# Optimization experiments

Measured on AMD Instinct MI355X. Metric: run time of the kernel, lower is better.

Reference implementation:

```python
import jax, jax.numpy as jnp
import numpy as np
from jax import lax

T = 3650      # days
H = 256       # MLP hidden width
N_IN = 4      # [s_snow, s_water, prcp, tmean]
N_OUT = 5     # [p_snow, p_rain, m, et, q]
DT = 1.0      # euler step (days), equals forcing sampling interval


def setup_inputs() -> dict:
    key = jax.random.key(0)
    ks = jax.random.split(key, 8)
    # inputs[:, 0]=s_snow init traj, [:,1]=s_water, [:,2]=prcp, [:,3]=tmean, [:,4]=time
    data = jax.random.normal(ks[0], (T, 4), dtype=jnp.float32)
    data = data.at[:, 2].set(jnp.abs(data[:, 2]))  # prcp >= 0
    time = jnp.arange(T, dtype=jnp.float32)[:, None]
    inputs = jnp.concatenate([data, time], axis=-1)  # [T, 5]
    dayl = jax.random.uniform(ks[1], (T,), dtype=jnp.float32)  # day length fraction
    s = 0.1  # small init keeps sinh/exp transforms stable over the long rollout
    W0 = jax.random.normal(ks[2], (N_IN, H), dtype=jnp.float32) * (s / np.sqrt(N_IN))
    b0 = jnp.zeros((H,), dtype=jnp.float32)
    W1 = jax.random.normal(ks[3], (H, H), dtype=jnp.float32) * (s / np.sqrt(H))
    b1 = jnp.zeros((H,), dtype=jnp.float32)
    W2 = jax.random.normal(ks[4], (H, H), dtype=jnp.float32) * (s / np.sqrt(H))
    b2 = jnp.zeros((H,), dtype=jnp.float32)
    Wout = jax.random.normal(ks[5], (H, N_OUT), dtype=jnp.float32) * (s / np.sqrt(H))
    bout = jnp.zeros((N_OUT,), dtype=jnp.float32)
    return {"inputs": inputs, "dayl": dayl, "W0": W0, "b0": b0, "W1": W1,
            "b1": b1, "W2": W2, "b2": b2, "Wout": Wout, "bout": bout}


def _step_function(x):
    return (jnp.tanh(5.0 * x) + 1.0) * 0.5


def reference(inputs, dayl, W0, b0, W1, b1, W2, b2, Wout, bout):
    prcp = inputs[:, 2]
    tmean = inputs[:, 3]
    s_snow0 = inputs[0, 0]
    s_water0 = inputs[0, 1]

    def mlp(x):  # x: [..., N_IN] -> [..., N_OUT]
        h = jnp.tanh(x @ W0 + b0)
        h = jnp.tanh(h @ W1 + b1)
        h = jnpp_tanh(h @ W2 + b2) if False else jnp.tanh(h @ W2 + b2)
        return h @ Wout + bout

    def derivs(s0, s1, p, tm, ld):
        o = mlp(jnp.stack([s0, s1, p, tm]))  # [5]
        p_snow, p_rain, m, et, q = o[0], o[1], o[2], o[3], o[4]
        # scale_target_vars transform path
        p_snow = jax.nn.relu(jnp.sinh(p_snow) * _step_function(-tm))
        p_rain = jax.nn.relu(jnp.sinh(p_rain))
        m = jax.nn.relu(_step_function(s0) * jnp.sinh(m))
        et = _step_function(s1) * jnp.exp(et) * ld
        q = _step_function(s1) * jnp.exp(q)
        return p_snow - m, p_rain + m - et - q

    def body(carry, xs):
        s0, s1 = carry
        p, tm, ld = xs
        d0, d1 = derivs(s0, s1, p, tm, ld)
        ns0 = s0 + DT * d0
        ns1 = s1 + DT * d1
        return (ns0, ns1), (ns0, ns1)

    xs = (prcp[:-1], tmean[:-1], dayl[:-1])
    _, (ss, sw) = lax.scan(body, (s_snow0, s_water0), xs)
    s_snow_nn = jnp.concatenate([s_snow0[None], ss])    # [T]
    s_water_nn = jnp.concatenate([s_water0[None], sw])  # [T]

    inputs_nn = jnp.stack([s_snow_nn, s_water_nn, prcp, tmean], axis=-1)  # [T, 4]
    q_output = mlp(inputs_nn)[:, -1]  # last head = q
    return (q_output, s_snow_nn, s_water_nn)
```

## Files before the change

### kernel.cpp

```cpp
#include <hip/hip_runtime.h>
#include <hip/hip_bf16.h>

#define TT 3650
#define HH 256

typedef _Float16 f16x4 __attribute__((ext_vector_type(4)));
typedef _Float16 f16x8 __attribute__((ext_vector_type(8)));
typedef float f32x4 __attribute__((ext_vector_type(4)));

__device__ __forceinline__ float xexp2(float x) { return __builtin_amdgcn_exp2f(x); }
__device__ __forceinline__ float xrcp(float x) { return __builtin_amdgcn_rcpf(x); }
__device__ __forceinline__ float xexp(float x) { return xexp2(x * 1.4426950408889634f); }
__device__ __forceinline__ float xtanh(float x) {
  float e = xexp2(x * 2.8853900817779268f);
  return 1.0f - 2.0f * xrcp(e + 1.0f);
}
__device__ __forceinline__ float xtanh_ds(float d) {
  float e = xexp2(d * 0.0028177637517362566f);
  return 1.0f - 2.0f * xrcp(e + 1.0f);
}
__device__ __forceinline__ float xstep(float x) {
  return xrcp(1.0f + xexp2(-14.426950408889634f * x));
}
__device__ __forceinline__ float xsinh(float x) {
  float e = xexp(x);
  return 0.5f * (e - xrcp(e));
}

#define DPPADD(x, ctrl)                                                        \
  (x) += __builtin_bit_cast(float, __builtin_amdgcn_update_dpp(                \
            0, __builtin_bit_cast(int, (x)), (ctrl), 0xf, 0xf, false));
#define RDLANE(x, l)                                                           \
  __builtin_bit_cast(float,                                                    \
      __builtin_amdgcn_readlane(__builtin_bit_cast(int, (x)), (l)))

#define REP8(M) M(0) M(1) M(2) M(3) M(4) M(5) M(6) M(7)
#define REPC(M) M(0) M(1) M(2) M(3)

#define WSCALE 1024.0f

#define SF_PAD 2

__global__ void __launch_bounds__(256, 1) exphydro_scan(
    const float* __restrict__ gin, const float* __restrict__ gdayl,
    const float* __restrict__ gW0, const float* __restrict__ gb0,
    const float* __restrict__ gW1, const float* __restrict__ gb1,
    const float* __restrict__ gW2, const float* __restrict__ gb2,
    const float* __restrict__ gWout, const float* __restrict__ gbout,
    float* __restrict__ gout) {
  __shared__ alignas(16) _Float16 h0l[HH];
  __shared__ alignas(16) _Float16 h1l[HH];
  __shared__ float sWP[64];
  __shared__ f32x4 sF[TT + SF_PAD];
  __shared__ float sQ[TT], sS0[TT], sS1[TT];

  const int tid = threadIdx.x;
  const int lane = tid & 63;
  const int w = tid >> 6;
  const int li = lane & 15;
  const int g = lane >> 4;
  const int jb = 64 * w + 4 * li;
  const int j0 = 64 * w + lane;

  for (int i = tid; i < TT; i += 256) {
    f32x4 F = {gin[5 * i + 2], gin[5 * i + 3], gdayl[i], 0.0f};
    sF[i] = F;
  }
  if (tid < SF_PAD) {
    f32x4 Z = {0.f, 0.f, 0.f, 0.f};
    sF[TT + tid] = Z;
  }
  if (tid < 64) sWP[tid] = 0.0f;

  float s0 = gin[0], s1 = gin[1];
  const float bo0 = gbout[0], bo1 = gbout[1], bo2 = gbout[2], bo3 = gbout[3],
              bo4 = gbout[4];
  const float w00J = gW0[j0], w01J = gW0[HH + j0], w02J = gW0[2 * HH + j0],
              w03J = gW0[3 * HH + j0], b0J = gb0[j0];
#define CDECL(c)                                                               \
  const float b1s_##c = gb1[jb + (c)] * WSCALE,                                \
              b2s_##c = gb2[jb + (c)] * WSCALE,                                \
              wo0_##c = gWout[5 * (jb + (c)) + 0],                             \
              wo1_##c = gWout[5 * (jb + (c)) + 1],                             \
              wo2_##c = gWout[5 * (jb + (c)) + 2],                             \
              wo3_##c = gWout[5 * (jb + (c)) + 3],                             \
              wo4_##c = gWout[5 * (jb + (c)) + 4];
  REPC(CDECL)
#undef CDECL

#define FDECL(i) f16x8 a1_0_##i, a1_1_##i, a1_2_##i, a1_3_##i,                 \
                       a2_0_##i, a2_1_##i, a2_2_##i, a2_3_##i;
  REP8(FDECL)
#undef FDECL
#define MK(dst, G, i, c)                                                       \
  {                                                                            \
    const float* p = (G) + (32 * (i) + g * 8) * HH + jb + (c);                 \
    f16x8 f;                                                                   \
    f[0] = (_Float16)(p[0] * WSCALE);      f[1] = (_Float16)(p[HH] * WSCALE);  \
    f[2] = (_Float16)(p[2 * HH] * WSCALE); f[3] = (_Float16)(p[3 * HH] * WSCALE); \
    f[4] = (_Float16)(p[4 * HH] * WSCALE); f[5] = (_Float16)(p[5 * HH] * WSCALE); \
    f[6] = (_Float16)(p[6 * HH] * WSCALE); f[7] = (_Float16)(p[7 * HH] * WSCALE); \
    dst = f;                                                                   \
    asm volatile("" : "+a"(dst));                                              \
  }
#define FINIT(i)                                                               \
  MK(a1_0_##i, gW1, i, 0) MK(a1_1_##i, gW1, i, 1)                              \
  MK(a1_2_##i, gW1, i, 2) MK(a1_3_##i, gW1, i, 3)                              \
  MK(a2_0_##i, gW2, i, 0) MK(a2_1_##i, gW2, i, 1)                              \
  MK(a2_2_##i, gW2, i, 2) MK(a2_3_##i, gW2, i, 3)
  REP8(FINIT)
#undef FINIT
#undef MK

  const char* hp0 = (const char*)h0l + g * 16;
  const char* hp1 = (const char*)h1l + g * 16;

#define MFMA(acc, a, b)                                                        \
  asm("v_mfma_f32_16x16x32_f16 %0, %1, %2, %0" : "+v"(acc) : "v"(a), "a"(b));

  __syncthreads();

  f32x4 Fc = sF[0];
  for (int t = 0; t < TT; ++t) {
    const float p_in = Fc[0];
    const float tm = Fc[1];
    const float ld = Fc[2];

    float h0J = xtanh(b0J + s0 * w00J + s1 * w01J + p_in * w02J + tm * w03J);
    h0l[j0] = (_Float16)h0J;
    __syncthreads();

    f32x4 Fn = sF[t + 1];

    f32x4 d0 = {b1s_0, 0.f, 0.f, 0.f}, d1 = {b1s_1, 0.f, 0.f, 0.f};
    f32x4 d2 = {b1s_2, 0.f, 0.f, 0.f}, d3 = {b1s_3, 0.f, 0.f, 0.f};
    asm volatile("s_nop 1" : "+v"(d0), "+v"(d1), "+v"(d2), "+v"(d3));
#define MM1(i)                                                                 \
  {                                                                            \
    f16x8 av = *(const f16x8*)(hp0 + (i) * 64);                                \
    MFMA(d0, av, a1_0_##i) MFMA(d1, av, a1_1_##i)                              \
    MFMA(d2, av, a1_2_##i) MFMA(d3, av, a1_3_##i)                              \
  }
    REP8(MM1)
#undef MM1
    asm volatile("s_nop 7\n\ts_nop 7" : "+v"(d0), "+v"(d1), "+v"(d2), "+v"(d3));
#define H1C(c) float h1_##c = xtanh_ds(d##c[0]);
    REPC(H1C)
#undef H1C
    if (lane < 16) {
      f16x4 hv = {(_Float16)h1_0, (_Float16)h1_1, (_Float16)h1_2,
                  (_Float16)h1_3};
      *(f16x4*)((char*)h1l + (jb << 1)) = hv;
    }
    __syncthreads();

    f32x4 e0 = {b2s_0, 0.f, 0.f, 0.f}, e1 = {b2s_1, 0.f, 0.f, 0.f};
    f32x4 e2 = {b2s_2, 0.f, 0.f, 0.f}, e3 = {b2s_3, 0.f, 0.f, 0.f};
    asm volatile("s_nop 1" : "+v"(e0), "+v"(e1), "+v"(e2), "+v"(e3));
#define MM2(i)                                                                 \
  {                                                                            \
    f16x8 av = *(const f16x8*)(hp1 + (i) * 64);                                \
    MFMA(e0, av, a2_0_##i) MFMA(e1, av, a2_1_##i)                              \
    MFMA(e2, av, a2_2_##i) MFMA(e3, av, a2_3_##i)                              \
  }
    REP8(MM2)
#undef MM2
    asm volatile("s_nop 7\n\ts_nop 7" : "+v"(e0), "+v"(e1), "+v"(e2), "+v"(e3));
#define H2C(c) float h2_##c = xtanh_ds(e##c[0]);
    REPC(H2C)
#undef H2C

    float p0 = h2_0 * wo0_0 + h2_1 * wo0_1 + h2_2 * wo0_2 + h2_3 * wo0_3;
    float p1 = h2_0 * wo1_0 + h2_1 * wo1_1 + h2_2 * wo1_2 + h2_3 * wo1_3;
    float p2 = h2_0 * wo2_0 + h2_1 * wo2_1 + h2_2 * wo2_2 + h2_3 * wo2_3;
    float p3 = h2_0 * wo3_0 + h2_1 * wo3_1 + h2_2 * wo3_2 + h2_3 * wo3_3;
    float p4 = h2_0 * wo4_0 + h2_1 * wo4_1 + h2_2 * wo4_2 + h2_3 * wo4_3;
    DPPADD(p0, 0x121) DPPADD(p0, 0x122) DPPADD(p0, 0x124) DPPADD(p0, 0x128)
    DPPADD(p1, 0x121) DPPADD(p1, 0x122) DPPADD(p1, 0x124) DPPADD(p1, 0x128)
    DPPADD(p2, 0x121) DPPADD(p2, 0x122) DPPADD(p2, 0x124) DPPADD(p2, 0x128)
    DPPADD(p3, 0x121) DPPADD(p3, 0x122) DPPADD(p3, 0x124) DPPADD(p3, 0x128)
    DPPADD(p4, 0x121) DPPADD(p4, 0x122) DPPADD(p4, 0x124) DPPADD(p4, 0x128)
    float pv = lane == 0 ? p0 : lane == 1 ? p1 : lane == 2 ? p2
                                          : lane == 3 ? p3 : p4;
    if (lane < 5) sWP[lane * 4 + w] = pv;
    __syncthreads();

    float v = sWP[lane];
    DPPADD(v, 0xB1)
    DPPADD(v, 0x4E)
    float o0 = RDLANE(v, 0) + bo0;
    float o1 = RDLANE(v, 4) + bo1;
    float o2 = RDLANE(v, 8) + bo2;
    float o3 = RDLANE(v, 12) + bo3;
    float o4 = RDLANE(v, 16) + bo4;
    if (tid == 64) {
      sQ[t] = o4;
      sS0[t] = s0;
      sS1[t] = s1;
    }
    float sh0 = xsinh(o0), sh1 = xsinh(o1), sh2 = xsinh(o2);
    float e3x = xexp(o3), e4x = xexp(o4);
    float stn = xstep(-tm), st0 = xstep(s0), st1 = xstep(s1);
    float psn = fmaxf(sh0 * stn, 0.0f);
    float prn = fmaxf(sh1, 0.0f);
    float mm = fmaxf(st0 * sh2, 0.0f);
    float evt = st1 * e3x * ld;
    float qq = st1 * e4x;
    s0 += psn - mm;
    s1 += prn + mm - evt - qq;
    Fc = Fn;
  }
#undef MFMA

  __syncthreads();
  for (int i = tid; i < TT; i += 256) {
    gout[i] = sQ[i];
    gout[TT + i] = sS0[i];
    gout[2 * TT + i] = sS1[i];
  }
}

extern "C" void kernel_launch(void* const* d_in, const int* in_sizes, int n_in,
                              void* d_out, int out_size, void* d_ws, size_t ws_size,
                              hipStream_t stream) {
  const float* gin   = (const float*)d_in[0];
  const float* gdayl = (const float*)d_in[1];
  const float* gW0   = (const float*)d_in[2];
  const float* gb0   = (const float*)d_in[3];
  const float* gW1   = (const float*)d_in[4];
  const float* gb1   = (const float*)d_in[5];
  const float* gW2   = (const float*)d_in[6];
  const float* gb2   = (const float*)d_in[7];
  const float* gWout = (const float*)d_in[8];
  const float* gbout = (const float*)d_in[9];
  float* gout = (float*)d_out;
  exphydro_scan<<<dim3(1), dim3(256), 0, stream>>>(
      gin, gdayl, gW0, gb0, gW1, gb1, gW2, gb2, gWout, gbout, gout);
}
```

Measured before the change: 4.591 ms.

## Split MLP K-reduction across 8 waves with LDS partial-sum exchange

Launches 512 threads and splits each hidden-layer matmul's K dimension between two wave halves. Each wave now holds half the weight fragments and issues 4 MFMAs per layer, and partial sums are exchanged through shared memory before tanh. This is meant to shorten the serial MFMA chain per time step. It adds two extra block-wide barriers and LDS round trips on every step of the sequential scan.

```diff
diff --git a/kernel.cpp b/kernel.cpp
--- a/kernel.cpp
+++ b/kernel.cpp
@@ -34,14 +34,13 @@
   __builtin_bit_cast(float,                                                    \
       __builtin_amdgcn_readlane(__builtin_bit_cast(int, (x)), (l)))
 
-#define REP8(M) M(0) M(1) M(2) M(3) M(4) M(5) M(6) M(7)
 #define REPC(M) M(0) M(1) M(2) M(3)
 
 #define WSCALE 1024.0f
 
 #define SF_PAD 2
 
-__global__ void __launch_bounds__(256, 1) exphydro_scan(
+__global__ void __launch_bounds__(512, 2) exphydro_scan(
     const float* __restrict__ gin, const float* __restrict__ gdayl,
     const float* __restrict__ gW0, const float* __restrict__ gb0,
     const float* __restrict__ gW1, const float* __restrict__ gb1,
@@ -50,6 +49,7 @@
     float* __restrict__ gout) {
   __shared__ alignas(16) _Float16 h0l[HH];
   __shared__ alignas(16) _Float16 h1l[HH];
+  __shared__ f32x4 sZ[8][16];
   __shared__ float sWP[64];
   __shared__ f32x4 sF[TT + SF_PAD];
   __shared__ float sQ[TT], sS0[TT], sS1[TT];
@@ -57,12 +57,15 @@
   const int tid = threadIdx.x;
   const int lane = tid & 63;
   const int w = tid >> 6;
+  const int jg = w & 3;
+  const int kh = w >> 2;
   const int li = lane & 15;
   const int g = lane >> 4;
-  const int jb = 64 * w + 4 * li;
-  const int j0 = 64 * w + lane;
-
-  for (int i = tid; i < TT; i += 256) {
+  const int jb = 64 * jg + 4 * li;
+  const int j0 = tid & 255;
+  const int sib = 4 * kh;
+
+  for (int i = tid; i < TT; i += 512) {
     f32x4 F = {gin[5 * i + 2], gin[5 * i + 3], gdayl[i], 0.0f};
     sF[i] = F;
   }
@@ -78,8 +81,8 @@
   const float w00J = gW0[j0], w01J = gW0[HH + j0], w02J = gW0[2 * HH + j0],
               w03J = gW0[3 * HH + j0], b0J = gb0[j0];
 #define CDECL(c)                                                               \
-  const float b1s_##c = gb1[jb + (c)] * WSCALE,                                \
-              b2s_##c = gb2[jb + (c)] * WSCALE,                                \
+  const float b1s_##c = kh ? 0.0f : gb1[jb + (c)] * WSCALE,                    \
+              b2s_##c = kh ? 0.0f : gb2[jb + (c)] * WSCALE,                    \
               wo0_##c = gWout[5 * (jb + (c)) + 0],                             \
               wo1_##c = gWout[5 * (jb + (c)) + 1],                             \
               wo2_##c = gWout[5 * (jb + (c)) + 2],                             \
@@ -90,11 +93,11 @@
 
 #define FDECL(i) f16x8 a1_0_##i, a1_1_##i, a1_2_##i, a1_3_##i,                 \
                        a2_0_##i, a2_1_##i, a2_2_##i, a2_3_##i;
-  REP8(FDECL)
+  REPC(FDECL)
 #undef FDECL
 #define MK(dst, G, i, c)                                                       \
   {                                                                            \
-    const float* p = (G) + (32 * (i) + g * 8) * HH + jb + (c);                 \
+    const float* p = (G) + (32 * (sib + (i)) + g * 8) * HH + jb + (c);         \
     f16x8 f;                                                                   \
     f[0] = (_Float16)(p[0] * WSCALE);      f[1] = (_Float16)(p[HH] * WSCALE);  \
     f[2] = (_Float16)(p[2 * HH] * WSCALE); f[3] = (_Float16)(p[3 * HH] * WSCALE); \
@@ -108,7 +111,7 @@
   MK(a1_2_##i, gW1, i, 2) MK(a1_3_##i, gW1, i, 3)                              \
   MK(a2_0_##i, gW2, i, 0) MK(a2_1_##i, gW2, i, 1)                              \
   MK(a2_2_##i, gW2, i, 2) MK(a2_3_##i, gW2, i, 3)
-  REP8(FINIT)
+  REPC(FINIT)
 #undef FINIT
 #undef MK
 
@@ -126,8 +129,10 @@
     const float tm = Fc[1];
     const float ld = Fc[2];
 
-    float h0J = xtanh(b0J + s0 * w00J + s1 * w01J + p_in * w02J + tm * w03J);
-    h0l[j0] = (_Float16)h0J;
+    if (kh == 0) {
+      float h0J = xtanh(b0J + s0 * w00J + s1 * w01J + p_in * w02J + tm * w03J);
+      h0l[j0] = (_Float16)h0J;
+    }
     __syncthreads();
 
     f32x4 Fn = sF[t + 1];
@@ -137,19 +142,24 @@
     asm volatile("s_nop 1" : "+v"(d0), "+v"(d1), "+v"(d2), "+v"(d3));
 #define MM1(i)                                                                 \
   {                                                                            \
-    f16x8 av = *(const f16x8*)(hp0 + (i) * 64);                                \
+    f16x8 av = *(const f16x8*)(hp0 + (sib + i) * 64);                          \
     MFMA(d0, av, a1_0_##i) MFMA(d1, av, a1_1_##i)                              \
     MFMA(d2, av, a1_2_##i) MFMA(d3, av, a1_3_##i)                              \
   }
-    REP8(MM1)
+    REPC(MM1)
 #undef MM1
     asm volatile("s_nop 7\n\ts_nop 7" : "+v"(d0), "+v"(d1), "+v"(d2), "+v"(d3));
-#define H1C(c) float h1_##c = xtanh_ds(d##c[0]);
-    REPC(H1C)
-#undef H1C
-    if (lane < 16) {
-      f16x4 hv = {(_Float16)h1_0, (_Float16)h1_1, (_Float16)h1_2,
-                  (_Float16)h1_3};
+    if (kh == 1 && lane < 16) {
+      f32x4 zp = {d0[0], d1[0], d2[0], d3[0]};
+      sZ[w][li] = zp;
+    }
+    __syncthreads();
+    if (kh == 0 && lane < 16) {
+      f32x4 zp = sZ[w + 4][li];
+      f16x4 hv = {(_Float16)xtanh_ds(d0[0] + zp[0]),
+                  (_Float16)xtanh_ds(d1[0] + zp[1]),
+                  (_Float16)xtanh_ds(d2[0] + zp[2]),
+                  (_Float16)xtanh_ds(d3[0] + zp[3])};
       *(f16x4*)((char*)h1l + (jb << 1)) = hv;
     }
     __syncthreads();
@@ -159,16 +169,23 @@
     asm volatile("s_nop 1" : "+v"(e0), "+v"(e1), "+v"(e2), "+v"(e3));
 #define MM2(i)                                                                 \
   {                                                                            \
-    f16x8 av = *(const f16x8*)(hp1 + (i) * 64);                                \
+    f16x8 av = *(const f16x8*)(hp1 + (sib + i) * 64);                          \
     MFMA(e0, av, a2_0_##i) MFMA(e1, av, a2_1_##i)                              \
     MFMA(e2, av, a2_2_##i) MFMA(e3, av, a2_3_##i)                              \
   }
-    REP8(MM2)
+    REPC(MM2)
 #undef MM2
     asm volatile("s_nop 7\n\ts_nop 7" : "+v"(e0), "+v"(e1), "+v"(e2), "+v"(e3));
-#define H2C(c) float h2_##c = xtanh_ds(e##c[0]);
-    REPC(H2C)
-#undef H2C
+    if (lane < 16) {
+      f32x4 zp = {e0[0], e1[0], e2[0], e3[0]};
+      sZ[w][li] = zp;
+    }
+    __syncthreads();
+    f32x4 zq = sZ[w ^ 4][li];
+    float h2_0 = xtanh_ds(e0[0] + zq[0]);
+    float h2_1 = xtanh_ds(e1[0] + zq[1]);
+    float h2_2 = xtanh_ds(e2[0] + zq[2]);
+    float h2_3 = xtanh_ds(e3[0] + zq[3]);
 
     float p0 = h2_0 * wo0_0 + h2_1 * wo0_1 + h2_2 * wo0_2 + h2_3 * wo0_3;
     float p1 = h2_0 * wo1_0 + h2_1 * wo1_1 + h2_2 * wo1_2 + h2_3 * wo1_3;
@@ -182,7 +199,7 @@
     DPPADD(p4, 0x121) DPPADD(p4, 0x122) DPPADD(p4, 0x124) DPPADD(p4, 0x128)
     float pv = lane == 0 ? p0 : lane == 1 ? p1 : lane == 2 ? p2
                                           : lane == 3 ? p3 : p4;
-    if (lane < 5) sWP[lane * 4 + w] = pv;
+    if (kh == 0 && lane < 5) sWP[lane * 4 + jg] = pv;
     __syncthreads();
 
     float v = sWP[lane];
@@ -213,7 +230,7 @@
 #undef MFMA
 
   __syncthreads();
-  for (int i = tid; i < TT; i += 256) {
+  for (int i = tid; i < TT; i += 512) {
     gout[i] = sQ[i];
     gout[TT + i] = sS0[i];
     gout[2 * TT + i] = sS1[i];
@@ -234,6 +251,6 @@
   const float* gWout = (const float*)d_in[8];
   const float* gbout = (const float*)d_in[9];
   float* gout = (float*)d_out;
-  exphydro_scan<<<dim3(1), dim3(256), 0, stream>>>(
+  exphydro_scan<<<dim3(1), dim3(512), 0, stream>>>(
       gin, gdayl, gW0, gb0, gW1, gb1, gW2, gb2, gWout, gbout, gout);
 }
```

Result: slower. 6.570 ms (+43.1%).
